# Kernel tuning notes

Measured on AMD Instinct MI355X. Metric: run time of the kernel, lower is better.

Reference implementation:

```python
import jax, jax.numpy as jnp
import numpy as np

R, S, RO, H, KD, VD = 14, 2, 7, 8, 32, 64  # resolution, stride, res_out, heads, key_dim, val_dim
EPS = 1e-5
SCALE = KD ** -0.5


def _bias_idxs():
    i = np.arange(R)
    kp = np.stack(np.meshgrid(i, i, indexing='ij')).reshape(2, -1)          # (2, 196)
    qi = np.arange(0, R, S)
    qp = np.stack(np.meshgrid(qi, qi, indexing='ij')).reshape(2, -1)        # (2, 49)
    rel = np.abs(qp[:, :, None] - kp[:, None, :])                           # (2, 49, 196)
    return jnp.asarray(rel[0] * R + rel[1], dtype=jnp.int32)                # (49, 196)

BIAS_IDXS = _bias_idxs()


def linear_norm(x, w, g, b, m, v):
    # Linear (no bias) followed by BatchNorm1d in eval mode (running stats)
    inv = g * jax.lax.rsqrt(v + EPS)
    return (x @ w.T) * inv + (b - m * inv)


def hardswish(x):
    return x * jnp.clip(x + 3.0, 0.0, 6.0) * (1.0 / 6.0)


def setup_inputs() -> dict:
    key = jax.random.key(0)
    ks = jax.random.split(key, 12)
    d = {
        'x': jax.random.normal(ks[0], (256, 196, 256), jnp.float32),
        'kv_w': jax.random.normal(ks[1], (768, 256), jnp.float32) * 0.02,
        'kv_g': jax.random.uniform(ks[2], (768,), jnp.float32, 0.5, 1.5),
        'kv_b': jax.random.normal(ks[3], (768,), jnp.float32) * 0.02,
        'kv_m': jax.random.normal(ks[4], (768,), jnp.float32) * 0.01,
        'kv_v': jax.random.uniform(ks[5], (768,), jnp.float32, 0.5, 1.5),
        'q_w': jax.random.normal(ks[6], (256, 256), jnp.float32) * 0.02,
        'q_g': jax.random.uniform(ks[7], (256,), jnp.float32, 0.5, 1.5),
        'q_b': jax.random.normal(ks[8], (256,), jnp.float32) * 0.02,
        'q_m': jax.random.normal(ks[9], (256,), jnp.float32) * 0.01,
        'q_v': jax.random.uniform(ks[10], (256,), jnp.float32, 0.5, 1.5),
        'proj_w': jax.random.normal(ks[11], (384, 512), jnp.float32) * 0.02,
        'proj_g': jnp.ones((384,), jnp.float32),
        'proj_b': jnp.zeros((384,), jnp.float32),
        'proj_m': jnp.zeros((384,), jnp.float32),
        'proj_v': jnp.ones((384,), jnp.float32),
        'attn_bias': jax.random.normal(jax.random.fold_in(key, 99), (H, R * R), jnp.float32) * 0.02,
    }
    return d


def reference(x, kv_w, kv_g, kv_b, kv_m, kv_v,
              q_w, q_g, q_b, q_m, q_v,
              proj_w, proj_g, proj_b, proj_m, proj_v, attn_bias):
    B, N, C = x.shape  # (B, 196, 256)
    kv = linear_norm(x, kv_w, kv_g, kv_b, kv_m, kv_v)          # (B, N, 768)
    kv = kv.reshape(B, N, H, KD + VD)                          # per-head split
    k = kv[..., :KD].transpose(0, 2, 3, 1)                     # (B, H, KD, N)
    v = kv[..., KD:].transpose(0, 2, 1, 3)                     # (B, H, N, VD)
    # Subsample queries on the 14x14 grid with stride 2 -> 49 tokens
    xq = x.reshape(B, R, R, C)[:, ::S, ::S].reshape(B, RO * RO, C)
    q = linear_norm(xq, q_w, q_g, q_b, q_m, q_v)               # (B, 49, 256)
    q = q.reshape(B, RO * RO, H, KD).transpose(0, 2, 1, 3)     # (B, H, 49, KD)
    bias = attn_bias[:, BIAS_IDXS]                             # (H, 49, 196)
    scores = jnp.einsum('bhqd,bhdn->bhqn', q, k) * SCALE + bias
    attn = jax.nn.softmax(scores, axis=-1)                     # (B, H, 49, 196)
    out = jnp.einsum('bhqn,bhnv->bhqv', attn, v)               # (B, H, 49, VD)
    out = out.transpose(0, 2, 1, 3).reshape(B, RO * RO, H * VD)  # (B, 49, 512)
    return linear_norm(hardswish(out), proj_w, proj_g, proj_b, proj_m, proj_v)  # (B, 49, 384)
```

## Files before the change

### kernel.cpp

```cpp
#include <hip/hip_runtime.h>

#define EPS 1e-5f
#define QK_SCALE 0.17677669529663687f

typedef __attribute__((ext_vector_type(8))) short bf16x8;
typedef __attribute__((ext_vector_type(4))) float f32x4;

__device__ inline unsigned short bf16_rne(float f) {
    unsigned int u = __float_as_uint(f);
    u = u + 0x7FFFu + ((u >> 16) & 1u);
    return (unsigned short)(u >> 16);
}
__device__ inline float bf16_f(unsigned short s) {
    return __uint_as_float(((unsigned int)s) << 16);
}
__device__ inline void split1(float v, unsigned short& hi, unsigned short& lo) {
    hi = bf16_rne(v); lo = bf16_rne(v - bf16_f(hi));
}

__device__ inline unsigned int cvtpk_bf16(float a, float b) {
    unsigned int r;
    asm("v_cvt_pk_bf16_f32 %0, %1, %2" : "=v"(r) : "v"(a), "v"(b));
    return r;
}
__device__ inline void split2pk(float a, float b, unsigned int& h, unsigned int& l) {
    h = cvtpk_bf16(a, b);
    float ra = a - __uint_as_float(h << 16);
    float rb = b - __uint_as_float(h & 0xFFFF0000u);
    l = cvtpk_bf16(ra, rb);
}
__device__ inline void split4pk(float4 v, uint2& h, uint2& l) {
    unsigned int h01, l01, h23, l23;
    split2pk(v.x, v.y, h01, l01);
    split2pk(v.z, v.w, h23, l23);
    h.x = h01; h.y = h23; l.x = l01; l.y = l23;
}

#define MFMA16(a, b, c) __builtin_amdgcn_mfma_f32_16x16x32_bf16((a), (b), (c), 0, 0, 0)

__global__ __launch_bounds__(256)
void prep_split(const float* __restrict__ kv_w, const float* __restrict__ q_w,
                const float* __restrict__ pw,
                unsigned short* __restrict__ wb_hi, unsigned short* __restrict__ wb_lo,
                unsigned short* __restrict__ pw_hi, unsigned short* __restrict__ pw_lo)
{
    int i = blockIdx.x * 256 + threadIdx.x;
    if (i < 262144) {
        int c = i & 255, j = (i >> 8) & 127, h = i >> 15;
        float v = (j < 96) ? kv_w[(h * 96 + j) * 256 + c]
                           : q_w[(h * 32 + (j - 96)) * 256 + c];
        unsigned short hi, lo; split1(v, hi, lo);
        wb_hi[i] = hi; wb_lo[i] = lo;
    } else {
        int p = i - 262144;
        if (p < 196608) {
            float v = pw[p];
            unsigned short hi, lo; split1(v, hi, lo);
            pw_hi[p] = hi; pw_lo[p] = lo;
        }
    }
}

__global__ __launch_bounds__(1024, 4)
void levit_fused_attn(const float* __restrict__ x,
                      const unsigned short* __restrict__ wb_hi,
                      const unsigned short* __restrict__ wb_lo,
                      const float* __restrict__ kv_g, const float* __restrict__ kv_b,
                      const float* __restrict__ kv_m, const float* __restrict__ kv_v,
                      const float* __restrict__ q_g, const float* __restrict__ q_b,
                      const float* __restrict__ q_m, const float* __restrict__ q_v,
                      const float* __restrict__ attn_bias,
                      unsigned short* __restrict__ ao_hi,
                      unsigned short* __restrict__ ao_lo)
{
    __shared__ __align__(16) unsigned short s_big[80192];
    __shared__ float bias_s[196];
    __shared__ float nrm_iv[128];
    __shared__ float nrm_be[128];

    unsigned short* s_phi = s_big;
    unsigned short* s_plo = s_big + 14848;
    unsigned short* s_khi = s_big + 29696;
    unsigned short* s_klo = s_big + 38016;
    unsigned short* s_qhi = s_big + 46336;
    unsigned short* s_qlo = s_big + 48416;
    unsigned short* s_vhi = s_big + 50496;
    unsigned short* s_vlo = s_big + 65344;
    unsigned short* st_xhi = s_big;
    unsigned short* st_xlo = s_big + 14976;
    unsigned short* st_whi = s_big + 29952;
    unsigned short* st_wlo = s_big + 39168;

    const int t = threadIdx.x;
    const int b = blockIdx.x;
    const int hh = blockIdx.y;

    const int l = t & 63;
    const int w = t >> 6;
    const int rg = w & 3;
    const int cg = w >> 2;
    const int lrow = l & 15;
    const int kg = (l >> 4) * 8;
    const int g4 = (l >> 4) * 4;

    const int wj = t >> 3, wc8 = (t & 7) * 8;
    const unsigned short* wsrc_hi = wb_hi + (hh * 128 + wj) * 256 + wc8;
    const unsigned short* wsrc_lo = wb_lo + (hh * 128 + wj) * 256 + wc8;
    const float* xbase = x + b * 196 * 256;
    const float4 f4z = {0.f, 0.f, 0.f, 0.f};

    float4 xr[4]; bf16x8 wrh, wrl;

    #pragma unroll
    for (int it = 0; it < 4; ++it) {
        const int f = t + 1024 * it;
        const int row = f >> 4, c4 = (f & 15) * 4;
        xr[it] = f4z;
        if (row < 196) xr[it] = *(const float4*)&xbase[row * 256 + c4];
    }
    wrh = *(const bf16x8*)&wsrc_hi[0];
    wrl = *(const bf16x8*)&wsrc_lo[0];

    if (t < 196) bias_s[t] = attn_bias[hh * 196 + t];
    if (t >= 256 && t < 384) {
        int jj = t - 256;
        float gg, bb, mm, vv;
        if (jj < 96) { int col = hh * 96 + jj;        gg = kv_g[col]; bb = kv_b[col]; mm = kv_m[col]; vv = kv_v[col]; }
        else         { int col = hh * 32 + (jj - 96); gg = q_g[col];  bb = q_b[col];  mm = q_m[col];  vv = q_v[col]; }
        float iv = gg * rsqrtf(vv + EPS);
        nrm_iv[jj] = iv; nrm_be[jj] = bb - mm * iv;
    }
    for (int i = t; i < 64 * 36; i += 1024) {
        int r = i / 36, c = 196 + i % 36;
        s_vhi[r * 232 + c] = 0; s_vlo[r * 232 + c] = 0;
    }

    f32x4 acc[4][2];
    #pragma unroll
    for (int i = 0; i < 4; ++i) { acc[i][0] = (f32x4){0,0,0,0}; acc[i][1] = (f32x4){0,0,0,0}; }

    #pragma unroll
    for (int it = 0; it < 4; ++it) {
        const int f = t + 1024 * it;
        const int row = f >> 4, c4 = (f & 15) * 4;
        if (row < 208) {
            uint2 h2, l2; split4pk(xr[it], h2, l2);
            *(uint2*)&st_xhi[row * 72 + c4] = h2;
            *(uint2*)&st_xlo[row * 72 + c4] = l2;
        }
    }
    *(bf16x8*)&st_whi[wj * 72 + wc8] = wrh;
    *(bf16x8*)&st_wlo[wj * 72 + wc8] = wrl;
    __syncthreads();

    for (int s = 0; s < 4; ++s) {
        if (s < 3) {
            const int kcn = 64 * (s + 1);
            #pragma unroll
            for (int it = 0; it < 4; ++it) {
                const int f = t + 1024 * it;
                const int row = f >> 4, c4 = (f & 15) * 4;
                xr[it] = f4z;
                if (row < 196) xr[it] = *(const float4*)&xbase[row * 256 + kcn + c4];
            }
            wrh = *(const bf16x8*)&wsrc_hi[kcn];
            wrl = *(const bf16x8*)&wsrc_lo[kcn];
        }

        #pragma unroll
        for (int sub = 0; sub < 2; ++sub) {
            const int ko = 32 * sub + kg;
            bf16x8 wfh[2], wfl[2];
            #pragma unroll
            for (int ctl = 0; ctl < 2; ++ctl) {
                const int jr = 16 * (2 * cg + ctl) + lrow;
                wfh[ctl] = *(const bf16x8*)&st_whi[jr * 72 + ko];
                wfl[ctl] = *(const bf16x8*)&st_wlo[jr * 72 + ko];
            }
            #pragma unroll
            for (int i = 0; i < 4; ++i) {
                const int rt = rg + 4 * i;
                if (rt < 13) {
                    const int arow = 16 * rt + lrow;
                    bf16x8 xh = *(const bf16x8*)&st_xhi[arow * 72 + ko];
                    bf16x8 xl = *(const bf16x8*)&st_xlo[arow * 72 + ko];
                    #pragma unroll
                    for (int ctl = 0; ctl < 2; ++ctl) {
                        acc[i][ctl] = MFMA16(wfh[ctl], xh, acc[i][ctl]);
                        acc[i][ctl] = MFMA16(wfh[ctl], xl, acc[i][ctl]);
                        acc[i][ctl] = MFMA16(wfl[ctl], xh, acc[i][ctl]);
                    }
                }
            }
        }

        if (s < 3) {
            __syncthreads();
            #pragma unroll
            for (int it = 0; it < 4; ++it) {
                const int f = t + 1024 * it;
                const int row = f >> 4, c4 = (f & 15) * 4;
                if (row < 208) {
                    uint2 h2, l2; split4pk(xr[it], h2, l2);
                    *(uint2*)&st_xhi[row * 72 + c4] = h2;
                    *(uint2*)&st_xlo[row * 72 + c4] = l2;
                }
            }
            *(bf16x8*)&st_whi[wj * 72 + wc8] = wrh;
            *(bf16x8*)&st_wlo[wj * 72 + wc8] = wrl;
            __syncthreads();
        }
    }
    __syncthreads();

    #pragma unroll
    for (int ctl = 0; ctl < 2; ++ctl) {
        const int ct = 2 * cg + ctl;
        const int j0 = 16 * ct + g4;
        const float iv0 = nrm_iv[j0+0], be0 = nrm_be[j0+0];
        const float iv1 = nrm_iv[j0+1], be1 = nrm_be[j0+1];
        const float iv2 = nrm_iv[j0+2], be2 = nrm_be[j0+2];
        const float iv3 = nrm_iv[j0+3], be3 = nrm_be[j0+3];
        #pragma unroll
        for (int i = 0; i < 4; ++i) {
            const int rt = rg + 4 * i;
            if (rt < 13) {
                const int n = 16 * rt + lrow;
                if (n < 196) {
                    float v0 = acc[i][ctl][0] * iv0 + be0;
                    float v1 = acc[i][ctl][1] * iv1 + be1;
                    float v2 = acc[i][ctl][2] * iv2 + be2;
                    float v3 = acc[i][ctl][3] * iv3 + be3;
                    unsigned int h01, l01, h23, l23;
                    split2pk(v0, v1, h01, l01);
                    split2pk(v2, v3, h23, l23);
                    if (ct < 2) {
                        *(uint2*)&s_khi[n * 40 + j0] = (uint2){h01, h23};
                        *(uint2*)&s_klo[n * 40 + j0] = (uint2){l01, l23};
                    } else if (ct < 6) {
                        const int vd0 = j0 - 32;
                        s_vhi[(vd0+0) * 232 + n] = (unsigned short)h01;
                        s_vhi[(vd0+1) * 232 + n] = (unsigned short)(h01 >> 16);
                        s_vhi[(vd0+2) * 232 + n] = (unsigned short)h23;
                        s_vhi[(vd0+3) * 232 + n] = (unsigned short)(h23 >> 16);
                        s_vlo[(vd0+0) * 232 + n] = (unsigned short)l01;
                        s_vlo[(vd0+1) * 232 + n] = (unsigned short)(l01 >> 16);
                        s_vlo[(vd0+2) * 232 + n] = (unsigned short)l23;
                        s_vlo[(vd0+3) * 232 + n] = (unsigned short)(l23 >> 16);
                    } else {
                        const int a = n / 28, rem = n - 28 * a;
                        if (rem < 14 && !(rem & 1)) {
                            const int qi = a * 7 + (rem >> 1);
                            *(uint2*)&s_qhi[qi * 40 + (j0 - 96)] = (uint2){h01, h23};
                            *(uint2*)&s_qlo[qi * 40 + (j0 - 96)] = (uint2){l01, l23};
                        }
                    }
                }
            }
        }
    }
    __syncthreads();

    for (int i = t; i < 64 * 24; i += 1024) {
        int r = i / 24, c = 208 + i % 24;
        s_phi[r * 232 + c] = 0; s_plo[r * 232 + c] = 0;
    }

    if (w < 4) {
        const int mt = w;
        bf16x8 qh = *(const bf16x8*)&s_qhi[(16 * mt + lrow) * 40 + kg];
        bf16x8 ql = *(const bf16x8*)&s_qlo[(16 * mt + lrow) * 40 + kg];
        f32x4 sv[13];
        #pragma unroll
        for (int nt = 0; nt < 13; ++nt) {
            bf16x8 kh = *(const bf16x8*)&s_khi[(16 * nt + lrow) * 40 + kg];
            bf16x8 kl = *(const bf16x8*)&s_klo[(16 * nt + lrow) * 40 + kg];
            f32x4 a = {0.f, 0.f, 0.f, 0.f};
            a = MFMA16(kh, qh, a);
            a = MFMA16(kh, ql, a);
            a = MFMA16(kl, qh, a);
            sv[nt] = a;
        }
        const int m = 16 * mt + lrow;
        const int mq = m < 49 ? m : 48;
        const int yq = (mq / 7) * 2, xq2 = (mq % 7) * 2;

        float lmax = -3.0e38f;
        #pragma unroll
        for (int nt = 0; nt < 13; ++nt) {
            #pragma unroll
            for (int reg = 0; reg < 4; ++reg) {
                const int n = 16 * nt + g4 + reg;
                float sc;
                if (n < 196) {
                    const int yk = n / 14, xk = n - 14 * yk;
                    int d0 = yq - yk;  d0 = d0 < 0 ? -d0 : d0;
                    int d1 = xq2 - xk; d1 = d1 < 0 ? -d1 : d1;
                    sc = sv[nt][reg] * QK_SCALE + bias_s[d0 * 14 + d1];
                } else {
                    sc = -1.0e30f;
                }
                sv[nt][reg] = sc;
                lmax = fmaxf(lmax, sc);
            }
        }
        lmax = fmaxf(lmax, __shfl_xor(lmax, 16, 64));
        lmax = fmaxf(lmax, __shfl_xor(lmax, 32, 64));
        float rsum = 0.f;
        #pragma unroll
        for (int nt = 0; nt < 13; ++nt)
            #pragma unroll
            for (int reg = 0; reg < 4; ++reg) {
                float p = __expf(sv[nt][reg] - lmax);
                sv[nt][reg] = p;
                rsum += p;
            }
        rsum += __shfl_xor(rsum, 16, 64);
        rsum += __shfl_xor(rsum, 32, 64);
        const float rinv = 1.f / rsum;
        #pragma unroll
        for (int nt = 0; nt < 13; ++nt) {
            unsigned int h01, l01, h23, l23;
            split2pk(sv[nt][0] * rinv, sv[nt][1] * rinv, h01, l01);
            split2pk(sv[nt][2] * rinv, sv[nt][3] * rinv, h23, l23);
            const int o = m * 232 + 16 * nt + g4;
            *(uint2*)&s_phi[o] = (uint2){h01, h23};
            *(uint2*)&s_plo[o] = (uint2){l01, l23};
        }
    }
    __syncthreads();

    {
        const int mtv = w & 3;
        const int ntv = w >> 2;
        f32x4 pacc = {0.f, 0.f, 0.f, 0.f};
        #pragma unroll
        for (int s = 0; s < 7; ++s) {
            bf16x8 ph = *(const bf16x8*)&s_phi[(16 * mtv + lrow) * 232 + 32 * s + kg];
            bf16x8 pl = *(const bf16x8*)&s_plo[(16 * mtv + lrow) * 232 + 32 * s + kg];
            bf16x8 vh = *(const bf16x8*)&s_vhi[(16 * ntv + lrow) * 232 + 32 * s + kg];
            bf16x8 vl = *(const bf16x8*)&s_vlo[(16 * ntv + lrow) * 232 + 32 * s + kg];
            pacc = MFMA16(vh, ph, pacc);
            pacc = MFMA16(vh, pl, pacc);
            pacc = MFMA16(vl, ph, pacc);
        }
        const int m = 16 * mtv + lrow;
        if (m < 49) {
            const int vd0 = 16 * ntv + g4;
            float hs0, hs1, hs2, hs3;
            { float v = pacc[0]; hs0 = v * fminf(fmaxf(v + 3.f, 0.f), 6.f) * (1.f/6.f); }
            { float v = pacc[1]; hs1 = v * fminf(fmaxf(v + 3.f, 0.f), 6.f) * (1.f/6.f); }
            { float v = pacc[2]; hs2 = v * fminf(fmaxf(v + 3.f, 0.f), 6.f) * (1.f/6.f); }
            { float v = pacc[3]; hs3 = v * fminf(fmaxf(v + 3.f, 0.f), 6.f) * (1.f/6.f); }
            unsigned int h01, l01, h23, l23;
            split2pk(hs0, hs1, h01, l01);
            split2pk(hs2, hs3, h23, l23);
            const int idx = ((b * 49 + m) * 8 + hh) * 64 + vd0;
            *(uint2*)&ao_hi[idx] = (uint2){h01, h23};
            *(uint2*)&ao_lo[idx] = (uint2){l01, l23};
        }
    }
}

__global__ __launch_bounds__(512, 6)
void levit_proj(const unsigned short* __restrict__ ao_hi,
                const unsigned short* __restrict__ ao_lo,
                const unsigned short* __restrict__ pw_hi,
                const unsigned short* __restrict__ pw_lo,
                const float* __restrict__ pg, const float* __restrict__ pb,
                const float* __restrict__ pm, const float* __restrict__ pv,
                float* __restrict__ out)
{
    __shared__ __align__(16) unsigned short s_a[2 * 64 * 72];
    __shared__ __align__(16) unsigned short s_w[2 * 96 * 72];

    unsigned short* s_ahi = s_a;          unsigned short* s_alo = s_a + 64 * 72;
    unsigned short* s_whi = s_w;          unsigned short* s_wlo = s_w + 96 * 72;

    const int t = threadIdx.x;
    const int b = blockIdx.x;
    const int cg = blockIdx.y;
    const int l = t & 63;
    const int w = t >> 6;
    const int lrow = l & 15;
    const int kg = (l >> 4) * 8;
    const int g4 = (l >> 4) * 4;

    const int ar = t >> 3, ac8 = (t & 7) * 8;
    const bool aval = (ar < 49);
    const long aoff = (long)(b * 49 + ar) * 512 + ac8;
    int wpl_[3], wr_[3], wc_[3];
    #pragma unroll
    for (int it = 0; it < 3; ++it) {
        int f = t + 512 * it;
        int plane = (f >= 768), rem = plane ? f - 768 : f;
        wpl_[it] = plane; wr_[it] = rem >> 3; wc_[it] = (rem & 7) * 8;
    }

    bf16x8 pa_h = {}, pa_l = {}, pwr[3];

    if (aval) {
        pa_h = *(const bf16x8*)&ao_hi[aoff];
        pa_l = *(const bf16x8*)&ao_lo[aoff];
    }
    #pragma unroll
    for (int it = 0; it < 3; ++it) {
        const unsigned short* src = wpl_[it] ? pw_lo : pw_hi;
        pwr[it] = *(const bf16x8*)&src[(cg * 96 + wr_[it]) * 512 + wc_[it]];
    }
    *(bf16x8*)&s_ahi[ar * 72 + ac8] = pa_h;
    *(bf16x8*)&s_alo[ar * 72 + ac8] = pa_l;
    #pragma unroll
    for (int it = 0; it < 3; ++it) {
        unsigned short* dst = wpl_[it] ? s_wlo : s_whi;
        *(bf16x8*)&dst[wr_[it] * 72 + wc_[it]] = pwr[it];
    }
    __syncthreads();

    const int mt = w & 3;
    const int ntb = 3 * (w >> 2);

    f32x4 acc[3] = {{0.f,0.f,0.f,0.f},{0.f,0.f,0.f,0.f},{0.f,0.f,0.f,0.f}};

    for (int s = 0; s < 8; ++s) {
        if (s < 7) {
            const int kc = 64 * (s + 1);
            pa_h = (bf16x8){}; pa_l = (bf16x8){};
            if (aval) {
                pa_h = *(const bf16x8*)&ao_hi[aoff + kc];
                pa_l = *(const bf16x8*)&ao_lo[aoff + kc];
            }
            #pragma unroll
            for (int it = 0; it < 3; ++it) {
                const unsigned short* src = wpl_[it] ? pw_lo : pw_hi;
                pwr[it] = *(const bf16x8*)&src[(cg * 96 + wr_[it]) * 512 + kc + wc_[it]];
            }
        }

        #pragma unroll
        for (int sub = 0; sub < 2; ++sub) {
            const int ko = 32 * sub + kg;
            bf16x8 ah = *(const bf16x8*)&s_ahi[(16 * mt + lrow) * 72 + ko];
            bf16x8 al = *(const bf16x8*)&s_alo[(16 * mt + lrow) * 72 + ko];
            #pragma unroll
            for (int i = 0; i < 3; ++i) {
                const int nt = ntb + i;
                bf16x8 bh = *(const bf16x8*)&s_whi[(16 * nt + lrow) * 72 + ko];
                bf16x8 bl = *(const bf16x8*)&s_wlo[(16 * nt + lrow) * 72 + ko];
                acc[i] = MFMA16(bh, ah, acc[i]);
                acc[i] = MFMA16(bl, ah, acc[i]);
                acc[i] = MFMA16(bh, al, acc[i]);
            }
        }

        if (s < 7) {
            __syncthreads();
            *(bf16x8*)&s_ahi[ar * 72 + ac8] = pa_h;
            *(bf16x8*)&s_alo[ar * 72 + ac8] = pa_l;
            #pragma unroll
            for (int it = 0; it < 3; ++it) {
                unsigned short* dst = wpl_[it] ? s_wlo : s_whi;
                *(bf16x8*)&dst[wr_[it] * 72 + wc_[it]] = pwr[it];
            }
            __syncthreads();
        }
    }

    const int r = 16 * mt + lrow;
    if (r < 49) {
        #pragma unroll
        for (int i = 0; i < 3; ++i) {
            const int nt = ntb + i;
            const int o0 = cg * 96 + 16 * nt + g4;
            const float4 g4v = *(const float4*)&pg[o0];
            const float4 v4v = *(const float4*)&pv[o0];
            const float4 b4v = *(const float4*)&pb[o0];
            const float4 m4v = *(const float4*)&pm[o0];
            float iv0 = g4v.x * rsqrtf(v4v.x + EPS);
            float iv1 = g4v.y * rsqrtf(v4v.y + EPS);
            float iv2 = g4v.z * rsqrtf(v4v.z + EPS);
            float iv3 = g4v.w * rsqrtf(v4v.w + EPS);
            float4 ov;
            ov.x = acc[i][0] * iv0 + (b4v.x - m4v.x * iv0);
            ov.y = acc[i][1] * iv1 + (b4v.y - m4v.y * iv1);
            ov.z = acc[i][2] * iv2 + (b4v.z - m4v.z * iv2);
            ov.w = acc[i][3] * iv3 + (b4v.w - m4v.w * iv3);
            *(float4*)&out[(b * 49 + r) * 384 + o0] = ov;
        }
    }
}

extern "C" void kernel_launch(void* const* d_in, const int* in_sizes, int n_in,
                              void* d_out, int out_size, void* d_ws, size_t ws_size,
                              hipStream_t stream) {
    const float* x     = (const float*)d_in[0];
    const float* kv_w  = (const float*)d_in[1];
    const float* kv_g  = (const float*)d_in[2];
    const float* kv_b  = (const float*)d_in[3];
    const float* kv_m  = (const float*)d_in[4];
    const float* kv_v  = (const float*)d_in[5];
    const float* q_wp  = (const float*)d_in[6];
    const float* q_g   = (const float*)d_in[7];
    const float* q_b   = (const float*)d_in[8];
    const float* q_m   = (const float*)d_in[9];
    const float* q_v   = (const float*)d_in[10];
    const float* pw    = (const float*)d_in[11];
    const float* pg    = (const float*)d_in[12];
    const float* pb    = (const float*)d_in[13];
    const float* pm    = (const float*)d_in[14];
    const float* pv    = (const float*)d_in[15];
    const float* ab    = (const float*)d_in[16];

    unsigned short* ao_hi = (unsigned short*)d_ws;
    unsigned short* ao_lo = ao_hi + 12544 * 512;
    unsigned short* wb_hi = ao_lo + 12544 * 512;
    unsigned short* wb_lo = wb_hi + 262144;
    unsigned short* pw_hi = wb_lo + 262144;
    unsigned short* pw_lo = pw_hi + 196608;

    prep_split<<<1792, 256, 0, stream>>>(kv_w, q_wp, pw, wb_hi, wb_lo, pw_hi, pw_lo);

    dim3 g1(256, 8);
    levit_fused_attn<<<g1, 1024, 0, stream>>>(x, wb_hi, wb_lo,
                                              kv_g, kv_b, kv_m, kv_v,
                                              q_g, q_b, q_m, q_v, ab, ao_hi, ao_lo);
    levit_proj<<<dim3(256, 4), 512, 0, stream>>>(ao_hi, ao_lo, pw_hi, pw_lo,
                                                 pg, pb, pm, pv, (float*)d_out);
}
```

Baseline: 284.8 us.

## Load weight MFMA fragments directly from global with register double-buffering

Weight fragments for the KV/Q projection GEMM are now loaded straight from global memory into registers in MFMA fragment layout, prefetched one k-substep ahead. This replaces staging the weights through shared memory, which removes LDS writes and reads and shrinks LDS traffic per stage. The bf16 split of x is also hoisted ahead of the barrier so the conversion overlaps with other waves finishing. In exchange it uses more registers, and the global reads are less coalesced because each lane fetches 16 bytes from strided rows.

Measured after the change: 333.9 us. 17.2% more time.

```diff
diff --git a/kernel.cpp b/kernel.cpp
--- a/kernel.cpp
+++ b/kernel.cpp
@@ -88,8 +88,6 @@
     unsigned short* s_vlo = s_big + 65344;
     unsigned short* st_xhi = s_big;
     unsigned short* st_xlo = s_big + 14976;
-    unsigned short* st_whi = s_big + 29952;
-    unsigned short* st_wlo = s_big + 39168;
 
     const int t = threadIdx.x;
     const int b = blockIdx.x;
@@ -103,13 +101,10 @@
     const int kg = (l >> 4) * 8;
     const int g4 = (l >> 4) * 4;
 
-    const int wj = t >> 3, wc8 = (t & 7) * 8;
-    const unsigned short* wsrc_hi = wb_hi + (hh * 128 + wj) * 256 + wc8;
-    const unsigned short* wsrc_lo = wb_lo + (hh * 128 + wj) * 256 + wc8;
     const float* xbase = x + b * 196 * 256;
     const float4 f4z = {0.f, 0.f, 0.f, 0.f};
 
-    float4 xr[4]; bf16x8 wrh, wrl;
+    float4 xr[4];
 
     #pragma unroll
     for (int it = 0; it < 4; ++it) {
@@ -118,8 +113,21 @@
         xr[it] = f4z;
         if (row < 196) xr[it] = *(const float4*)&xbase[row * 256 + c4];
     }
-    wrh = *(const bf16x8*)&wsrc_hi[0];
-    wrl = *(const bf16x8*)&wsrc_lo[0];
+
+    const unsigned short* wfsrc_hi[2];
+    const unsigned short* wfsrc_lo[2];
+    #pragma unroll
+    for (int ctl = 0; ctl < 2; ++ctl) {
+        const int jr = 16 * (2 * cg + ctl) + lrow;
+        wfsrc_hi[ctl] = wb_hi + (hh * 128 + jr) * 256 + kg;
+        wfsrc_lo[ctl] = wb_lo + (hh * 128 + jr) * 256 + kg;
+    }
+    bf16x8 wfh[2][2], wfl[2][2];
+    #pragma unroll
+    for (int ctl = 0; ctl < 2; ++ctl) {
+        wfh[0][ctl] = *(const bf16x8*)&wfsrc_hi[ctl][0];
+        wfl[0][ctl] = *(const bf16x8*)&wfsrc_lo[ctl][0];
+    }
 
     if (t < 196) bias_s[t] = attn_bias[hh * 196 + t];
     if (t >= 256 && t < 384) {
@@ -149,8 +157,6 @@
             *(uint2*)&st_xlo[row * 72 + c4] = l2;
         }
     }
-    *(bf16x8*)&st_whi[wj * 72 + wc8] = wrh;
-    *(bf16x8*)&st_wlo[wj * 72 + wc8] = wrl;
     __syncthreads();
 
     for (int s = 0; s < 4; ++s) {
@@ -163,20 +169,22 @@
                 xr[it] = f4z;
                 if (row < 196) xr[it] = *(const float4*)&xbase[row * 256 + kcn + c4];
             }
-            wrh = *(const bf16x8*)&wsrc_hi[kcn];
-            wrl = *(const bf16x8*)&wsrc_lo[kcn];
         }
 
         #pragma unroll
         for (int sub = 0; sub < 2; ++sub) {
+            const int u = 2 * s + sub;
+            const int cur = sub;
+            const int nxt = sub ^ 1;
+            if (u < 7) {
+                const int kon = 32 * (u + 1);
+                #pragma unroll
+                for (int ctl = 0; ctl < 2; ++ctl) {
+                    wfh[nxt][ctl] = *(const bf16x8*)&wfsrc_hi[ctl][kon];
+                    wfl[nxt][ctl] = *(const bf16x8*)&wfsrc_lo[ctl][kon];
+                }
+            }
             const int ko = 32 * sub + kg;
-            bf16x8 wfh[2], wfl[2];
-            #pragma unroll
-            for (int ctl = 0; ctl < 2; ++ctl) {
-                const int jr = 16 * (2 * cg + ctl) + lrow;
-                wfh[ctl] = *(const bf16x8*)&st_whi[jr * 72 + ko];
-                wfl[ctl] = *(const bf16x8*)&st_wlo[jr * 72 + ko];
-            }
             #pragma unroll
             for (int i = 0; i < 4; ++i) {
                 const int rt = rg + 4 * i;
@@ -186,28 +194,28 @@
                     bf16x8 xl = *(const bf16x8*)&st_xlo[arow * 72 + ko];
                     #pragma unroll
                     for (int ctl = 0; ctl < 2; ++ctl) {
-                        acc[i][ctl] = MFMA16(wfh[ctl], xh, acc[i][ctl]);
-                        acc[i][ctl] = MFMA16(wfh[ctl], xl, acc[i][ctl]);
-                        acc[i][ctl] = MFMA16(wfl[ctl], xh, acc[i][ctl]);
+                        acc[i][ctl] = MFMA16(wfh[cur][ctl], xh, acc[i][ctl]);
+                        acc[i][ctl] = MFMA16(wfh[cur][ctl], xl, acc[i][ctl]);
+                        acc[i][ctl] = MFMA16(wfl[cur][ctl], xh, acc[i][ctl]);
                     }
                 }
             }
         }
 
         if (s < 3) {
+            uint2 xh2[4], xl2[4];
+            #pragma unroll
+            for (int it = 0; it < 4; ++it) split4pk(xr[it], xh2[it], xl2[it]);
             __syncthreads();
             #pragma unroll
             for (int it = 0; it < 4; ++it) {
                 const int f = t + 1024 * it;
                 const int row = f >> 4, c4 = (f & 15) * 4;
                 if (row < 208) {
-                    uint2 h2, l2; split4pk(xr[it], h2, l2);
-                    *(uint2*)&st_xhi[row * 72 + c4] = h2;
-                    *(uint2*)&st_xlo[row * 72 + c4] = l2;
+                    *(uint2*)&st_xhi[row * 72 + c4] = xh2[it];
+                    *(uint2*)&st_xlo[row * 72 + c4] = xl2[it];
                 }
             }
-            *(bf16x8*)&st_whi[wj * 72 + wc8] = wrh;
-            *(bf16x8*)&st_wlo[wj * 72 + wc8] = wrl;
             __syncthreads();
         }
     }
```

## Double-buffer KV/Q projection staging with 32-wide K slices and prefetch V fragments

Applied to the files above, without the earlier changes.

Replaces the single-buffered 64-wide K-chunk staging of x and weight tiles with two LDS buffers of 32-wide slices, so the next slice is written while the current one is consumed. This halves the barriers per slice. It also prefetches V fragments into registers during the softmax phase and moves the zero-padding of V and P into otherwise idle waves. In exchange it adds more loop iterations, extra live registers for the prefetched V fragments, and tighter LDS aliasing with the later attention buffers.

Result: no change. 286.3 us (+0.5%).

```diff
diff --git a/kernel.cpp b/kernel.cpp
--- a/kernel.cpp
+++ b/kernel.cpp
@@ -86,10 +86,14 @@
     unsigned short* s_qlo = s_big + 48416;
     unsigned short* s_vhi = s_big + 50496;
     unsigned short* s_vlo = s_big + 65344;
-    unsigned short* st_xhi = s_big;
-    unsigned short* st_xlo = s_big + 14976;
-    unsigned short* st_whi = s_big + 29952;
-    unsigned short* st_wlo = s_big + 39168;
+    unsigned short* bx_hi0 = s_big;
+    unsigned short* bx_lo0 = s_big + 8320;
+    unsigned short* bx_hi1 = s_big + 29696;
+    unsigned short* bx_lo1 = s_big + 38016;
+    unsigned short* bw_hi0 = s_big + 50496;
+    unsigned short* bw_lo0 = s_big + 55616;
+    unsigned short* bw_hi1 = s_big + 60736;
+    unsigned short* bw_lo1 = s_big + 65856;
 
     const int t = threadIdx.x;
     const int b = blockIdx.x;
@@ -103,23 +107,25 @@
     const int kg = (l >> 4) * 8;
     const int g4 = (l >> 4) * 4;
 
-    const int wj = t >> 3, wc8 = (t & 7) * 8;
-    const unsigned short* wsrc_hi = wb_hi + (hh * 128 + wj) * 256 + wc8;
-    const unsigned short* wsrc_lo = wb_lo + (hh * 128 + wj) * 256 + wc8;
+    const bool xact = (t < 832);
+    const int xrow = t >> 2, xc8 = (t & 3) * 8;
+    const int wpl = t >> 9, wrow = (t & 511) >> 2, wc8 = (t & 3) * 8;
+    const unsigned short* wsrc = (wpl ? wb_lo : wb_hi) + (hh * 128 + wrow) * 256 + wc8;
     const float* xbase = x + b * 196 * 256;
     const float4 f4z = {0.f, 0.f, 0.f, 0.f};
 
-    float4 xr[4]; bf16x8 wrh, wrl;
-
-    #pragma unroll
-    for (int it = 0; it < 4; ++it) {
-        const int f = t + 1024 * it;
-        const int row = f >> 4, c4 = (f & 15) * 4;
-        xr[it] = f4z;
-        if (row < 196) xr[it] = *(const float4*)&xbase[row * 256 + c4];
-    }
-    wrh = *(const bf16x8*)&wsrc_hi[0];
-    wrl = *(const bf16x8*)&wsrc_lo[0];
+    float4 xa[2], xb[2]; bf16x8 wr[2];
+
+    #pragma unroll
+    for (int sl = 0; sl < 2; ++sl) {
+        const int kc = 32 * sl;
+        xa[sl] = f4z; xb[sl] = f4z;
+        if (xact && xrow < 196) {
+            xa[sl] = *(const float4*)&xbase[xrow * 256 + kc + xc8];
+            xb[sl] = *(const float4*)&xbase[xrow * 256 + kc + xc8 + 4];
+        }
+        wr[sl] = *(const bf16x8*)&wsrc[kc];
+    }
 
     if (t < 196) bias_s[t] = attn_bias[hh * 196 + t];
     if (t >= 256 && t < 384) {
@@ -130,60 +136,56 @@
         float iv = gg * rsqrtf(vv + EPS);
         nrm_iv[jj] = iv; nrm_be[jj] = bb - mm * iv;
     }
-    for (int i = t; i < 64 * 36; i += 1024) {
-        int r = i / 36, c = 196 + i % 36;
-        s_vhi[r * 232 + c] = 0; s_vlo[r * 232 + c] = 0;
-    }
 
     f32x4 acc[4][2];
     #pragma unroll
     for (int i = 0; i < 4; ++i) { acc[i][0] = (f32x4){0,0,0,0}; acc[i][1] = (f32x4){0,0,0,0}; }
 
-    #pragma unroll
-    for (int it = 0; it < 4; ++it) {
-        const int f = t + 1024 * it;
-        const int row = f >> 4, c4 = (f & 15) * 4;
-        if (row < 208) {
-            uint2 h2, l2; split4pk(xr[it], h2, l2);
-            *(uint2*)&st_xhi[row * 72 + c4] = h2;
-            *(uint2*)&st_xlo[row * 72 + c4] = l2;
-        }
-    }
-    *(bf16x8*)&st_whi[wj * 72 + wc8] = wrh;
-    *(bf16x8*)&st_wlo[wj * 72 + wc8] = wrl;
+    if (xact) {
+        uint2 ha, la, hb, lb;
+        split4pk(xa[0], ha, la); split4pk(xb[0], hb, lb);
+        *(uint4*)&bx_hi0[xrow * 40 + xc8] = (uint4){ha.x, ha.y, hb.x, hb.y};
+        *(uint4*)&bx_lo0[xrow * 40 + xc8] = (uint4){la.x, la.y, lb.x, lb.y};
+    }
+    {
+        unsigned short* wd = wpl ? bw_lo0 : bw_hi0;
+        *(bf16x8*)&wd[wrow * 40 + wc8] = wr[0];
+    }
     __syncthreads();
 
-    for (int s = 0; s < 4; ++s) {
-        if (s < 3) {
-            const int kcn = 64 * (s + 1);
-            #pragma unroll
-            for (int it = 0; it < 4; ++it) {
-                const int f = t + 1024 * it;
-                const int row = f >> 4, c4 = (f & 15) * 4;
-                xr[it] = f4z;
-                if (row < 196) xr[it] = *(const float4*)&xbase[row * 256 + kcn + c4];
-            }
-            wrh = *(const bf16x8*)&wsrc_hi[kcn];
-            wrl = *(const bf16x8*)&wsrc_lo[kcn];
-        }
-
-        #pragma unroll
-        for (int sub = 0; sub < 2; ++sub) {
-            const int ko = 32 * sub + kg;
+    #pragma unroll
+    for (int s = 0; s < 8; ++s) {
+        const int p = s & 1;
+        unsigned short* cx_hi = p ? bx_hi1 : bx_hi0;
+        unsigned short* cx_lo = p ? bx_lo1 : bx_lo0;
+        unsigned short* cw_hi = p ? bw_hi1 : bw_hi0;
+        unsigned short* cw_lo = p ? bw_lo1 : bw_lo0;
+
+        if (s < 6) {
+            const int kc = 32 * (s + 2);
+            xa[p] = f4z; xb[p] = f4z;
+            if (xact && xrow < 196) {
+                xa[p] = *(const float4*)&xbase[xrow * 256 + kc + xc8];
+                xb[p] = *(const float4*)&xbase[xrow * 256 + kc + xc8 + 4];
+            }
+            wr[p] = *(const bf16x8*)&wsrc[kc];
+        }
+
+        {
             bf16x8 wfh[2], wfl[2];
             #pragma unroll
             for (int ctl = 0; ctl < 2; ++ctl) {
                 const int jr = 16 * (2 * cg + ctl) + lrow;
-                wfh[ctl] = *(const bf16x8*)&st_whi[jr * 72 + ko];
-                wfl[ctl] = *(const bf16x8*)&st_wlo[jr * 72 + ko];
+                wfh[ctl] = *(const bf16x8*)&cw_hi[jr * 40 + kg];
+                wfl[ctl] = *(const bf16x8*)&cw_lo[jr * 40 + kg];
             }
             #pragma unroll
             for (int i = 0; i < 4; ++i) {
                 const int rt = rg + 4 * i;
                 if (rt < 13) {
                     const int arow = 16 * rt + lrow;
-                    bf16x8 xh = *(const bf16x8*)&st_xhi[arow * 72 + ko];
-                    bf16x8 xl = *(const bf16x8*)&st_xlo[arow * 72 + ko];
+                    bf16x8 xh = *(const bf16x8*)&cx_hi[arow * 40 + kg];
+                    bf16x8 xl = *(const bf16x8*)&cx_lo[arow * 40 + kg];
                     #pragma unroll
                     for (int ctl = 0; ctl < 2; ++ctl) {
                         acc[i][ctl] = MFMA16(wfh[ctl], xh, acc[i][ctl]);
@@ -194,24 +196,22 @@
             }
         }
 
-        if (s < 3) {
-            __syncthreads();
-            #pragma unroll
-            for (int it = 0; it < 4; ++it) {
-                const int f = t + 1024 * it;
-                const int row = f >> 4, c4 = (f & 15) * 4;
-                if (row < 208) {
-                    uint2 h2, l2; split4pk(xr[it], h2, l2);
-                    *(uint2*)&st_xhi[row * 72 + c4] = h2;
-                    *(uint2*)&st_xlo[row * 72 + c4] = l2;
-                }
-            }
-            *(bf16x8*)&st_whi[wj * 72 + wc8] = wrh;
-            *(bf16x8*)&st_wlo[wj * 72 + wc8] = wrl;
-            __syncthreads();
-        }
-    }
-    __syncthreads();
+        if (s < 7) {
+            unsigned short* nx_hi = p ? bx_hi0 : bx_hi1;
+            unsigned short* nx_lo = p ? bx_lo0 : bx_lo1;
+            unsigned short* nw_hi = p ? bw_hi0 : bw_hi1;
+            unsigned short* nw_lo = p ? bw_lo0 : bw_lo1;
+            if (xact) {
+                uint2 ha, la, hb, lb;
+                split4pk(xa[p ^ 1], ha, la); split4pk(xb[p ^ 1], hb, lb);
+                *(uint4*)&nx_hi[xrow * 40 + xc8] = (uint4){ha.x, ha.y, hb.x, hb.y};
+                *(uint4*)&nx_lo[xrow * 40 + xc8] = (uint4){la.x, la.y, lb.x, lb.y};
+            }
+            unsigned short* wd = wpl ? nw_lo : nw_hi;
+            *(bf16x8*)&wd[wrow * 40 + wc8] = wr[p ^ 1];
+        }
+        __syncthreads();
+    }
 
     #pragma unroll
     for (int ctl = 0; ctl < 2; ++ctl) {
@@ -259,12 +259,15 @@
             }
         }
     }
+    for (int i = t; i < 64 * 36; i += 1024) {
+        int r = i / 36, c = 196 + i % 36;
+        s_vhi[r * 232 + c] = 0; s_vlo[r * 232 + c] = 0;
+    }
     __syncthreads();
 
-    for (int i = t; i < 64 * 24; i += 1024) {
-        int r = i / 24, c = 208 + i % 24;
-        s_phi[r * 232 + c] = 0; s_plo[r * 232 + c] = 0;
-    }
+    const int mtv = w & 3;
+    const int ntv = w >> 2;
+    bf16x8 vph[7], vpl[7];
 
     if (w < 4) {
         const int mt = w;
@@ -327,22 +330,33 @@
             *(uint2*)&s_phi[o] = (uint2){h01, h23};
             *(uint2*)&s_plo[o] = (uint2){l01, l23};
         }
+        #pragma unroll
+        for (int s = 0; s < 7; ++s) {
+            vph[s] = *(const bf16x8*)&s_vhi[(16 * ntv + lrow) * 232 + 32 * s + kg];
+            vpl[s] = *(const bf16x8*)&s_vlo[(16 * ntv + lrow) * 232 + 32 * s + kg];
+        }
+    } else {
+        for (int i = t - 256; i < 64 * 24; i += 768) {
+            int r = i / 24, c = 208 + i % 24;
+            s_phi[r * 232 + c] = 0; s_plo[r * 232 + c] = 0;
+        }
+        #pragma unroll
+        for (int s = 0; s < 7; ++s) {
+            vph[s] = *(const bf16x8*)&s_vhi[(16 * ntv + lrow) * 232 + 32 * s + kg];
+            vpl[s] = *(const bf16x8*)&s_vlo[(16 * ntv + lrow) * 232 + 32 * s + kg];
+        }
     }
     __syncthreads();
 
     {
-        const int mtv = w & 3;
-        const int ntv = w >> 2;
         f32x4 pacc = {0.f, 0.f, 0.f, 0.f};
         #pragma unroll
         for (int s = 0; s < 7; ++s) {
             bf16x8 ph = *(const bf16x8*)&s_phi[(16 * mtv + lrow) * 232 + 32 * s + kg];
             bf16x8 pl = *(const bf16x8*)&s_plo[(16 * mtv + lrow) * 232 + 32 * s + kg];
-            bf16x8 vh = *(const bf16x8*)&s_vhi[(16 * ntv + lrow) * 232 + 32 * s + kg];
-            bf16x8 vl = *(const bf16x8*)&s_vlo[(16 * ntv + lrow) * 232 + 32 * s + kg];
-            pacc = MFMA16(vh, ph, pacc);
-            pacc = MFMA16(vh, pl, pacc);
-            pacc = MFMA16(vl, ph, pacc);
+            pacc = MFMA16(vph[s], ph, pacc);
+            pacc = MFMA16(vph[s], pl, pacc);
+            pacc = MFMA16(vpl[s], ph, pacc);
         }
         const int m = 16 * mtv + lrow;
         if (m < 49) {
```
